# Kernel optimization log

Measured on AMD Instinct MI355X. Metric: run time of the kernel, lower is better.

## Reference

```python
import jax, jax.numpy as jnp
import numpy as np

HEADS = 8
DIM_HEAD = 64


def setup_inputs() -> dict:
    key = jax.random.key(0)
    ks = jax.random.split(key, 6)
    B, Nq, Nk, Dq = 4, 2048, 2048, 1024
    inner = HEADS * DIM_HEAD  # 512
    return {
        "x": jax.random.normal(ks[0], (B, Nq, Dq), jnp.float32),
        "context": jax.random.normal(ks[1], (B, Nk, Dq), jnp.float32),
        "Wq": jax.random.normal(ks[2], (Dq, inner), jnp.float32) * 0.02,
        "Wkv": jax.random.normal(ks[3], (Dq, 2 * inner), jnp.float32) * 0.02,
        "Wout": jax.random.normal(ks[4], (inner, Dq), jnp.float32) * 0.02,
        "bout": jax.random.normal(ks[5], (Dq,), jnp.float32) * 0.02,
        "topk": 64,
    }


def reference(x, context, Wq, Wkv, Wout, bout, topk):
    B, Nq, _ = x.shape
    Nk = context.shape[1]
    H, D = HEADS, DIM_HEAD
    scale = D ** -0.5

    # projections: b n (h d) -> b h n d
    q = (x @ Wq).reshape(B, Nq, H, D).transpose(0, 2, 1, 3)
    kv = context @ Wkv
    k, v = jnp.split(kv, 2, axis=-1)
    k = k.reshape(B, Nk, H, D).transpose(0, 2, 1, 3)
    v = v.reshape(B, Nk, H, D).transpose(0, 2, 1, 3)

    sim = jnp.einsum('bhid,bhjd->bhij', q, k) * scale  # [B,H,Nq,Nk]

    # top-k sparsification: keep only topk keys per query, mask rest to -max
    k_eff = min(int(topk), Nk)
    _, idx = jax.lax.top_k(sim, k_eff)  # [B,H,Nq,k_eff]
    keep = jnp.zeros(sim.shape, dtype=bool)
    bi = jnp.arange(B)[:, None, None, None]
    hi = jnp.arange(H)[None, :, None, None]
    qi = jnp.arange(Nq)[None, None, :, None]
    keep = keep.at[bi, hi, qi, idx].set(True)
    max_neg = -jnp.finfo(sim.dtype).max
    sim = jnp.where(keep, sim, max_neg)

    attn = jax.nn.softmax(sim, axis=-1)
    out = jnp.einsum('bhij,bhjd->bhid', attn, v)
    out = out.transpose(0, 2, 1, 3).reshape(B, Nq, H * D)
    return out @ Wout + bout
```

## Files before the change

kernel.cpp:

```cpp
#include <hip/hip_runtime.h>
#include <math.h>

#define BATCH 4
#define NQ 2048
#define NK 2048
#define DQ 1024
#define NHEADS 8
#define DHEAD 64
#define INNER (NHEADS*DHEAD)
#define NROWS (BATCH*NHEADS*NQ)
#define CAND_MAX 128

using frag_ab = __attribute__((ext_vector_type(8))) short;
using frag_cd = __attribute__((ext_vector_type(4))) float;
using u16x8   = __attribute__((ext_vector_type(8))) unsigned short;

static __device__ __forceinline__ unsigned short f32_to_bf16_rne(float f) {
  unsigned u = __float_as_uint(f);
  u += 0x7FFFu + ((u >> 16) & 1u);
  return (unsigned short)(u >> 16);
}

static __device__ __forceinline__ void split_trunc(float f, unsigned short& h, unsigned short& l) {
  unsigned u = __float_as_uint(f);
  h = (unsigned short)(u >> 16);
  float hf = __uint_as_float(u & 0xFFFF0000u);
  unsigned r = __float_as_uint(f - hf);
  l = (unsigned short)(r >> 16);
}

static __device__ __forceinline__ void split3(float f, unsigned short& h,
                                              unsigned short& m, unsigned short& l) {
  unsigned u = __float_as_uint(f);
  h = (unsigned short)(u >> 16);
  float hf = __uint_as_float(u & 0xFFFF0000u);
  float r1 = f - hf;
  unsigned u1 = __float_as_uint(r1);
  m = (unsigned short)(u1 >> 16);
  float mf = __uint_as_float(u1 & 0xFFFF0000u);
  float r2 = r1 - mf;
  l = (unsigned short)(__float_as_uint(r2) >> 16);
}

__global__ __launch_bounds__(256) void split_wT3(
    const float* __restrict__ W, int ldw, int coloff, int K, int N,
    unsigned short* __restrict__ TH, unsigned short* __restrict__ TM,
    unsigned short* __restrict__ TL)
{
  __shared__ float tile[32*33];
  const int k0 = blockIdx.x * 32, n0 = blockIdx.y * 32;
  const int t = threadIdx.x;
  {
    int lk = t >> 3, ln4 = (t & 7) * 4;
    const float4 v = *(const float4*)(W + (size_t)(k0 + lk)*ldw + coloff + n0 + ln4);
    tile[lk*33 + ln4+0] = v.x;
    tile[lk*33 + ln4+1] = v.y;
    tile[lk*33 + ln4+2] = v.z;
    tile[lk*33 + ln4+3] = v.w;
  }
  __syncthreads();
  int n = t >> 3, k4 = (t & 7) * 4;
  #pragma unroll
  for (int j = 0; j < 4; ++j) {
    unsigned short h, m, l;
    split3(tile[(k4+j)*33 + n], h, m, l);
    size_t o = (size_t)(n0 + n)*K + k0 + k4 + j;
    TH[o] = h; TM[o] = m; TL[o] = l;
  }
}

__global__ __launch_bounds__(256) void split_wT(
    const float* __restrict__ W, int ldw, int coloff, int K, int N,
    unsigned short* __restrict__ TH, unsigned short* __restrict__ TL)
{
  __shared__ float tile[32*33];
  const int k0 = blockIdx.x * 32, n0 = blockIdx.y * 32;
  const int t = threadIdx.x;
  {
    int lk = t >> 3, ln4 = (t & 7) * 4;
    const float4 v = *(const float4*)(W + (size_t)(k0 + lk)*ldw + coloff + n0 + ln4);
    tile[lk*33 + ln4+0] = v.x;
    tile[lk*33 + ln4+1] = v.y;
    tile[lk*33 + ln4+2] = v.z;
    tile[lk*33 + ln4+3] = v.w;
  }
  __syncthreads();
  int n = t >> 3, k4 = (t & 7) * 4;
  #pragma unroll
  for (int j = 0; j < 4; ++j) {
    unsigned short h, l;
    split_trunc(tile[(k4+j)*33 + n], h, l);
    TH[(size_t)(n0 + n)*K + k0 + k4 + j] = h;
    TL[(size_t)(n0 + n)*K + k0 + k4 + j] = l;
  }
}

__global__ __launch_bounds__(256) void gemm_mfma6_proj(
    const float* __restrict__ A,
    const unsigned short* __restrict__ BtH, const unsigned short* __restrict__ BtM,
    const unsigned short* __restrict__ BtL,
    float* __restrict__ C32,
    unsigned short* __restrict__ Hi, unsigned short* __restrict__ Lo)
{
  extern __shared__ unsigned short smp[];
  unsigned short* ah = smp;
  unsigned short* am = ah + 128*72;
  unsigned short* al = am + 128*72;
  unsigned short* bh = al + 128*72;
  unsigned short* bm = bh + 128*72;
  unsigned short* bl = bm + 128*72;

  const int t = threadIdx.x;
  const int w = t >> 6, l = t & 63;
  const int lr = l & 15, quad = l >> 4;
  const int n0 = blockIdx.x * 128, m0 = blockIdx.y * 128;

  frag_cd acc[2][8];
  #pragma unroll
  for (int ms = 0; ms < 2; ++ms)
    #pragma unroll
    for (int nt = 0; nt < 8; ++nt)
      acc[ms][nt] = (frag_cd){0.f, 0.f, 0.f, 0.f};

  for (int kt = 0; kt < DQ; kt += 64) {
    #pragma unroll
    for (int i = 0; i < 4; ++i) {
      int idx = i*256 + t;
      int row = idx >> 3, k8 = (idx & 7) * 8;
      const float* src = A + (size_t)(m0 + row) * DQ + kt + k8;
      float4 v0 = *(const float4*)(src);
      float4 v1 = *(const float4*)(src + 4);
      float vv[8] = {v0.x, v0.y, v0.z, v0.w, v1.x, v1.y, v1.z, v1.w};
      unsigned short h8[8], m8[8], l8[8];
      #pragma unroll
      for (int j = 0; j < 8; ++j) split3(vv[j], h8[j], m8[j], l8[j]);
      *(u16x8*)(ah + row*72 + k8) = *(u16x8*)h8;
      *(u16x8*)(am + row*72 + k8) = *(u16x8*)m8;
      *(u16x8*)(al + row*72 + k8) = *(u16x8*)l8;
    }
    #pragma unroll
    for (int i = 0; i < 4; ++i) {
      int idx = i*256 + t;
      int n = idx >> 3, k8 = (idx & 7) * 8;
      size_t o = (size_t)(n0 + n)*DQ + kt + k8;
      *(u16x8*)(bh + n*72 + k8) = *(const u16x8*)(BtH + o);
      *(u16x8*)(bm + n*72 + k8) = *(const u16x8*)(BtM + o);
      *(u16x8*)(bl + n*72 + k8) = *(const u16x8*)(BtL + o);
    }
    __syncthreads();
    #pragma unroll
    for (int ks = 0; ks < 2; ++ks) {
      frag_ab aH[2], aM[2], aL[2];
      #pragma unroll
      for (int ms = 0; ms < 2; ++ms) {
        int row = w*32 + ms*16 + lr;
        aH[ms] = *(const frag_ab*)(ah + row*72 + ks*32 + quad*8);
        aM[ms] = *(const frag_ab*)(am + row*72 + ks*32 + quad*8);
        aL[ms] = *(const frag_ab*)(al + row*72 + ks*32 + quad*8);
      }
      #pragma unroll
      for (int nt = 0; nt < 8; ++nt) {
        int bn = nt*16 + lr;
        frag_ab bH_ = *(const frag_ab*)(bh + bn*72 + ks*32 + quad*8);
        frag_ab bM_ = *(const frag_ab*)(bm + bn*72 + ks*32 + quad*8);
        frag_ab bL_ = *(const frag_ab*)(bl + bn*72 + ks*32 + quad*8);
        #pragma unroll
        for (int ms = 0; ms < 2; ++ms) {
          frag_cd c = acc[ms][nt];
          c = __builtin_amdgcn_mfma_f32_16x16x32_bf16(aL[ms], bH_, c, 0, 0, 0);
          c = __builtin_amdgcn_mfma_f32_16x16x32_bf16(aH[ms], bL_, c, 0, 0, 0);
          c = __builtin_amdgcn_mfma_f32_16x16x32_bf16(aM[ms], bM_, c, 0, 0, 0);
          c = __builtin_amdgcn_mfma_f32_16x16x32_bf16(aM[ms], bH_, c, 0, 0, 0);
          c = __builtin_amdgcn_mfma_f32_16x16x32_bf16(aH[ms], bM_, c, 0, 0, 0);
          c = __builtin_amdgcn_mfma_f32_16x16x32_bf16(aH[ms], bH_, c, 0, 0, 0);
          acc[ms][nt] = c;
        }
      }
    }
    __syncthreads();
  }

  #pragma unroll
  for (int ms = 0; ms < 2; ++ms)
    #pragma unroll
    for (int nt = 0; nt < 8; ++nt) {
      int cc = n0 + nt*16 + lr;
      int h = cc >> 6, d = cc & 63;
      #pragma unroll
      for (int i = 0; i < 4; ++i) {
        int r = m0 + w*32 + ms*16 + quad*4 + i;
        int b = r >> 11, n = r & (NQ - 1);
        size_t idx = (((size_t)(b*NHEADS + h))*NQ + n)*64 + d;
        float vf = acc[ms][nt][i];
        C32[idx] = vf;
        unsigned short hb = f32_to_bf16_rne(vf);
        float hf = __uint_as_float((unsigned)hb << 16);
        unsigned short lb = f32_to_bf16_rne(vf - hf);
        Hi[idx] = hb;
        Lo[idx] = lb;
      }
    }
}

template<int MODE>
__global__ __launch_bounds__(256) void gemm_mfma3(
    const float* __restrict__ A, int lda,
    const unsigned short* __restrict__ BtH, const unsigned short* __restrict__ BtL,
    int K, int N, const float* __restrict__ bias, float* __restrict__ C0)
{
  __shared__ unsigned short ah[128*72];
  __shared__ unsigned short al[128*72];
  __shared__ unsigned short bh2[64*72];
  __shared__ unsigned short bl2[64*72];
  const int t = threadIdx.x;
  const int w = t >> 6, l = t & 63;
  const int lr = l & 15, quad = l >> 4;
  const int n0 = blockIdx.x * 64, m0 = blockIdx.y * 128;

  frag_cd acc[2][4];
  #pragma unroll
  for (int ms = 0; ms < 2; ++ms)
    #pragma unroll
    for (int nt = 0; nt < 4; ++nt)
      acc[ms][nt] = (frag_cd){0.f, 0.f, 0.f, 0.f};

  for (int kt = 0; kt < K; kt += 64) {
    #pragma unroll
    for (int i = 0; i < 4; ++i) {
      int idx = i*256 + t;
      int row = idx >> 3, k8 = (idx & 7) * 8;
      const float* src = A + (size_t)(m0 + row) * lda + kt + k8;
      float4 v0 = *(const float4*)(src);
      float4 v1 = *(const float4*)(src + 4);
      float vv[8] = {v0.x, v0.y, v0.z, v0.w, v1.x, v1.y, v1.z, v1.w};
      unsigned short h8[8], l8[8];
      #pragma unroll
      for (int j = 0; j < 8; ++j) split_trunc(vv[j], h8[j], l8[j]);
      *(u16x8*)(ah + row*72 + k8) = *(u16x8*)h8;
      *(u16x8*)(al + row*72 + k8) = *(u16x8*)l8;
    }
    #pragma unroll
    for (int i = 0; i < 2; ++i) {
      int idx = i*256 + t;
      int n = idx >> 3, k8 = (idx & 7) * 8;
      *(u16x8*)(bh2 + n*72 + k8) = *(const u16x8*)(BtH + (size_t)(n0 + n)*K + kt + k8);
      *(u16x8*)(bl2 + n*72 + k8) = *(const u16x8*)(BtL + (size_t)(n0 + n)*K + kt + k8);
    }
    __syncthreads();
    #pragma unroll
    for (int ks = 0; ks < 2; ++ks) {
      frag_ab aH[2], aL[2], bH[4], bL[4];
      #pragma unroll
      for (int ms = 0; ms < 2; ++ms) {
        int row = w*32 + ms*16 + lr;
        aH[ms] = *(const frag_ab*)(ah + row*72 + ks*32 + quad*8);
        aL[ms] = *(const frag_ab*)(al + row*72 + ks*32 + quad*8);
      }
      #pragma unroll
      for (int nt = 0; nt < 4; ++nt) {
        int row = nt*16 + lr;
        bH[nt] = *(const frag_ab*)(bh2 + row*72 + ks*32 + quad*8);
        bL[nt] = *(const frag_ab*)(bl2 + row*72 + ks*32 + quad*8);
      }
      #pragma unroll
      for (int ms = 0; ms < 2; ++ms)
        #pragma unroll
        for (int nt = 0; nt < 4; ++nt) {
          acc[ms][nt] = __builtin_amdgcn_mfma_f32_16x16x32_bf16(aH[ms], bH[nt], acc[ms][nt], 0, 0, 0);
          acc[ms][nt] = __builtin_amdgcn_mfma_f32_16x16x32_bf16(aH[ms], bL[nt], acc[ms][nt], 0, 0, 0);
          acc[ms][nt] = __builtin_amdgcn_mfma_f32_16x16x32_bf16(aL[ms], bH[nt], acc[ms][nt], 0, 0, 0);
        }
    }
    __syncthreads();
  }

  #pragma unroll
  for (int ms = 0; ms < 2; ++ms)
    #pragma unroll
    for (int nt = 0; nt < 4; ++nt) {
      int cc = n0 + nt*16 + lr;
      #pragma unroll
      for (int i = 0; i < 4; ++i) {
        int r = m0 + w*32 + ms*16 + quad*4 + i;
        float v = acc[ms][nt][i];
        if (MODE == 0) {
          C0[(size_t)r * N + cc] = v + bias[cc];
        } else {
          int b = r >> 11, n = r & (NQ - 1);
          int h = cc >> 6, d = cc & 63;
          C0[(((size_t)(b*NHEADS + h))*NK + n)*64 + d] = v;
        }
      }
    }
}

__global__ __launch_bounds__(256) void score_mfma(
    const unsigned short* __restrict__ Qhi, const unsigned short* __restrict__ Qlo,
    const unsigned short* __restrict__ Khi, const unsigned short* __restrict__ Klo,
    unsigned short* __restrict__ S16, int bh0)
{
  extern __shared__ unsigned short sm[];
  unsigned short* qh = sm;
  unsigned short* ql = qh + 128*72;
  unsigned short* kh = ql + 128*72;
  unsigned short* kl = kh + 128*72;

  const int t  = threadIdx.x;
  const int qt = blockIdx.x, kt = blockIdx.y;
  const int bh = bh0 + blockIdx.z;
  const size_t qbase = ((size_t)bh*NQ + qt*128) * 64;
  const size_t kbase = ((size_t)bh*NK + kt*128) * 64;

  #pragma unroll
  for (int i = 0; i < 4; ++i) {
    int c   = t + i*256;
    int row = c >> 3, off = (c & 7) * 8;
    *(u16x8*)(qh + row*72 + off) = *(const u16x8*)(Qhi + qbase + row*64 + off);
    *(u16x8*)(ql + row*72 + off) = *(const u16x8*)(Qlo + qbase + row*64 + off);
    *(u16x8*)(kh + row*72 + off) = *(const u16x8*)(Khi + kbase + row*64 + off);
    *(u16x8*)(kl + row*72 + off) = *(const u16x8*)(Klo + kbase + row*64 + off);
  }
  __syncthreads();

  const int w = t >> 6, l = t & 63;
  const int quad = l >> 4, lr = l & 15;

  frag_ab aH[2][2], aL[2][2];
  #pragma unroll
  for (int qs = 0; qs < 2; ++qs) {
    int row = w*32 + qs*16 + lr;
    #pragma unroll
    for (int s = 0; s < 2; ++s) {
      aH[qs][s] = *(const frag_ab*)(qh + row*72 + s*32 + quad*8);
      aL[qs][s] = *(const frag_ab*)(ql + row*72 + s*32 + quad*8);
    }
  }

  for (int ks = 0; ks < 8; ++ks) {
    frag_ab bH[2], bL[2];
    int krow = ks*16 + lr;
    #pragma unroll
    for (int s = 0; s < 2; ++s) {
      bH[s] = *(const frag_ab*)(kh + krow*72 + s*32 + quad*8);
      bL[s] = *(const frag_ab*)(kl + krow*72 + s*32 + quad*8);
    }
    #pragma unroll
    for (int qs = 0; qs < 2; ++qs) {
      frag_cd c = {0.f, 0.f, 0.f, 0.f};
      #pragma unroll
      for (int s = 0; s < 2; ++s) {
        c = __builtin_amdgcn_mfma_f32_16x16x32_bf16(aH[qs][s], bH[s], c, 0, 0, 0);
        c = __builtin_amdgcn_mfma_f32_16x16x32_bf16(aH[qs][s], bL[s], c, 0, 0, 0);
        c = __builtin_amdgcn_mfma_f32_16x16x32_bf16(aL[qs][s], bH[s], c, 0, 0, 0);
      }
      int qrow = qt*128 + w*32 + qs*16 + quad*4;
      int kcol = kt*128 + ks*16 + lr;
      size_t base = ((size_t)blockIdx.z * NQ + qrow) * NK + kcol;
      #pragma unroll
      for (int i = 0; i < 4; ++i) {
        _Float16 h = (_Float16)(c[i] * 0.125f);
        S16[base + (size_t)i*NK] = __builtin_bit_cast(unsigned short, h);
      }
    }
  }
}

__global__ __launch_bounds__(256) void select_rows(
    const unsigned short* __restrict__ S16, unsigned short* __restrict__ cand,
    int* __restrict__ cnt, const int* __restrict__ topkp, int row0)
{
  const int t = threadIdx.x;
  const int w = t >> 6, l = t & 63;
  const int rl = blockIdx.x * 4 + w;
  const size_t row = (size_t)row0 + rl;
  const unsigned short* Sr = S16 + (size_t)rl * NK;
  const unsigned long long lmask = (1ull << l) - 1ull;

  int kEff = *topkp;
  if (kEff > CAND_MAX) kEff = CAND_MAX;
  if (kEff < 1) kEff = 1;

  unsigned uv[32];
  #pragma unroll
  for (int c = 0; c < 32; ++c) {
    unsigned bb = Sr[c*64 + l];
    uv[c] = (bb & 0x8000u) ? (~bb & 0xFFFFu) : (bb | 0x8000u);
  }
  unsigned lo_ = 0u, hi_ = 0xFFFFu;
  while (lo_ < hi_) {
    unsigned mid = (lo_ + hi_ + 1u) >> 1;
    int c_ = 0;
    #pragma unroll
    for (int c = 0; c < 32; ++c) c_ += (uv[c] >= mid) ? 1 : 0;
    #pragma unroll
    for (int off = 32; off > 0; off >>= 1) c_ += __shfl_xor(c_, off);
    if (c_ >= kEff) lo_ = mid; else hi_ = mid - 1;
  }
  unsigned short sb = (lo_ & 0x8000u) ? (unsigned short)(lo_ & 0x7FFFu)
                                      : (unsigned short)(~lo_ & 0xFFFFu);
  float skth = (float)__builtin_bit_cast(_Float16, sb);
  float smarg = skth - 3e-3f;
  _Float16 hm = (_Float16)smarg;
  unsigned short mb = __builtin_bit_cast(unsigned short, hm);
  unsigned um = (mb & 0x8000u) ? (~(unsigned)mb & 0xFFFFu) : ((unsigned)mb | 0x8000u);

  int base = 0;
  for (int c = 0; c < 32; ++c) {
    bool pred = (uv[c] >= um);
    unsigned long long msk = __ballot(pred);
    if (pred) {
      int pos = base + __popcll(msk & lmask);
      if (pos < CAND_MAX) cand[row*CAND_MAX + pos] = (unsigned short)(c*64 + l);
    }
    base += __popcll(msk);
  }
  if (l == 0) cnt[row] = (base < CAND_MAX) ? base : CAND_MAX;
}

__global__ __launch_bounds__(256) void attn_phase_b(
    const float* __restrict__ Q32, const float* __restrict__ K32,
    const float* __restrict__ V32, const unsigned short* __restrict__ cand,
    const int* __restrict__ cnt, float* __restrict__ inner,
    const int* __restrict__ topkp)
{
  __shared__ uint2 pvbuf[4][128];

  const int t = threadIdx.x;
  const int w = t >> 6, l = t & 63;
  const int nwg = (int)gridDim.x;
  const int bid = (int)blockIdx.x;
  const int swz = (bid & 7) * (nwg >> 3) + (bid >> 3);
  const size_t row = (size_t)swz * 4 + w;
  const int bh = (int)(row >> 11);
  const int q  = (int)(row & (NQ - 1));
  const unsigned long long lmask = (1ull << l) - 1ull;

  int kEff = *topkp;
  if (kEff > CAND_MAX) kEff = CAND_MAX;
  if (kEff < 1) kEff = 1;
  int m = cnt[row];
  if (kEff > m) kEff = m;

  const float* Kb = K32 + (size_t)bh * NK * 64;
  const float* Vb = V32 + (size_t)bh * NK * 64;

  const int g = l >> 3, r = l & 7;
  double2 q2[4];
  #pragma unroll
  for (int i = 0; i < 4; ++i) {
    float2 qf = *(const float2*)(Q32 + row*64 + i*16 + r*2);
    q2[i].x = (double)qf.x;
    q2[i].y = (double)qf.y;
  }

  int ck[2];
  ck[0] = cand[row*CAND_MAX + l];
  ck[1] = cand[row*CAND_MAX + 64 + l];
  double cs[2] = {-INFINITY, -INFINITY};
  unsigned long long cu[2] = {0ull, 0ull};

  #define RESCORE_PASS(P, C)                                                  \
  {                                                                           \
    const int j = (P)*8 + g;                                                  \
    const bool valid = (j < m);                                               \
    int key = __shfl(ck[C], j & 63);                                          \
    const float* kp = Kb + (size_t)(valid ? key : 0) * 64;                    \
    double s0 = 0.0, s1 = 0.0;                                                \
    _Pragma("unroll")                                                         \
    for (int i = 0; i < 4; ++i) {                                             \
      float2 kv = *(const float2*)(kp + i*16 + r*2);                          \
      s0 = fma((double)kv.x, q2[i].x, s0);                                    \
      s1 = fma((double)kv.y, q2[i].y, s1);                                    \
    }                                                                         \
    double s = s0 + s1;                                                       \
    s += __shfl_xor(s, 1);                                                    \
    s += __shfl_xor(s, 2);                                                    \
    s += __shfl_xor(s, 4);                                                    \
    s *= 0.125;                                                               \
    double sc = __shfl(s, (l & 7) * 8);                                       \
    const int pp = (P) & 7;                                                   \
    if ((l >> 3) == pp && ((C)*64 + pp*8 + (l & 7)) < m) {                    \
      unsigned long long b = (unsigned long long)__double_as_longlong(sc);    \
      cs[C] = sc;                                                             \
      cu[C] = (b >> 63) ? ~b : (b | 0x8000000000000000ull);                   \
    }                                                                         \
  }

  if (m <= 64) {
    #pragma unroll
    for (int p = 0; p < 8; ++p) RESCORE_PASS(p, 0)
  } else {
    #pragma unroll
    for (int p = 0; p < 8; ++p) RESCORE_PASS(p, 0)
    const int np2 = 8 + ((m - 64 + 7) >> 3);
    for (int p = 8; p < np2; ++p) RESCORE_PASS(p, 1)
  }
  #undef RESCORE_PASS

  const unsigned hu0 = (unsigned)(cu[0] >> 32), lu0 = (unsigned)cu[0];
  const unsigned hu1 = (unsigned)(cu[1] >> 32), lu1 = (unsigned)cu[1];

  unsigned T32 = 0u;
  for (int bit = 31; bit >= 0; --bit) {
    unsigned cT = T32 | (1u << bit);
    int tot = __popcll(__ballot(hu0 >= cT)) + __popcll(__ballot(hu1 >= cT));
    if (tot >= kEff) T32 = cT;
  }
  unsigned Tlo;
  {
    int cgt32 = __popcll(__ballot(hu0 > T32)) + __popcll(__ballot(hu1 > T32));
    bool e0 = (hu0 == T32), e1 = (hu1 == T32);
    unsigned long long bm0 = __ballot(e0), bm1 = __ballot(e1);
    int ceq = __popcll(bm0) + __popcll(bm1);
    int nEq32 = kEff - cgt32;
    if (ceq == 1) {
      Tlo = bm0 ? __shfl(lu0, (int)__builtin_ctzll(bm0))
                : __shfl(lu1, (int)__builtin_ctzll(bm1));
    } else {
      unsigned TL = 0u;
      for (int bit = 31; bit >= 0; --bit) {
        unsigned cT = TL | (1u << bit);
        int tot = __popcll(__ballot(e0 && lu0 >= cT))
                + __popcll(__ballot(e1 && lu1 >= cT));
        if (tot >= nEq32) TL = cT;
      }
      Tlo = TL;
    }
  }
  const unsigned long long T = ((unsigned long long)T32 << 32) | Tlo;

  double s_kth;
  { unsigned long long bb = (T >> 63) ? (T & 0x7FFFFFFFFFFFFFFFull) : ~T;
    s_kth = __longlong_as_double((long long)bb); }

  double nx = -INFINITY;
  #pragma unroll
  for (int c = 0; c < 2; ++c) { double v = (cu[c] < T) ? cs[c] : -INFINITY; nx = fmax(nx, v); }
  #pragma unroll
  for (int off = 32; off > 0; off >>= 1) nx = fmax(nx, __shfl_xor(nx, off));

  double smax = fmax(cs[0], cs[1]);
  #pragma unroll
  for (int off = 32; off > 0; off >>= 1) smax = fmax(smax, __shfl_xor(smax, off));

  const double DELTA = 5e-6;
  float wgt[2];
  if (!(s_kth - nx < 2.0*DELTA)) {
    int cgt = __popcll(__ballot(cu[0] > T)) + __popcll(__ballot(cu[1] > T));
    int nEq = kEff - cgt;
    int eqBase = 0;
    #pragma unroll
    for (int c = 0; c < 2; ++c) {
      bool eq = (cu[c] == T);
      unsigned long long eqm = __ballot(eq);
      int er = __popcll(eqm & lmask);
      bool sel = (cu[c] > T) || (eq && (eqBase + er) < nEq);
      eqBase += __popcll(eqm);
      wgt[c] = sel ? expf((float)(cs[c] - smax)) : 0.f;
    }
  } else {
    double cmid = 0.5 * (s_kth + nx);
    #pragma unroll
    for (int c = 0; c < 2; ++c) {
      double mu = 0.5 + (cs[c] - cmid) / (2.0*DELTA);
      mu = fmin(1.0, fmax(0.0, mu));
      wgt[c] = (float)mu * expf((float)(cs[c] - smax));
    }
  }

  pvbuf[w][l]      = make_uint2((unsigned)ck[0] & (NK - 1), __float_as_uint(wgt[0]));
  pvbuf[w][64 + l] = make_uint2((unsigned)ck[1] & (NK - 1), __float_as_uint(wgt[1]));
  float wsum = wgt[0] + wgt[1];
  #pragma unroll
  for (int off = 32; off > 0; off >>= 1) wsum += __shfl_xor(wsum, off);
  asm volatile("s_waitcnt lgkmcnt(0)" ::: "memory");

  const int sub = l >> 4;
  const int dl  = l & 15;
  const float* Vb4 = Vb + dl * 4;
  float ax = 0.f, ay = 0.f, az = 0.f, aw = 0.f;
  const int mm4 = (m + 3) & ~3;
  #pragma unroll 4
  for (int j0 = 0; j0 < mm4; j0 += 4) {
    uint2 p = pvbuf[w][j0 + sub];
    float wj = __uint_as_float(p.y);
    const float4 v = *(const float4*)(Vb4 + ((size_t)p.x << 6));
    ax = fmaf(wj, v.x, ax);
    ay = fmaf(wj, v.y, ay);
    az = fmaf(wj, v.z, az);
    aw = fmaf(wj, v.w, aw);
  }
  #pragma unroll
  for (int off = 32; off >= 16; off >>= 1) {
    ax += __shfl_xor(ax, off);
    ay += __shfl_xor(ay, off);
    az += __shfl_xor(az, off);
    aw += __shfl_xor(aw, off);
  }
  if (sub == 0) {
    int b = bh >> 3, h = bh & 7;
    float inv = 1.0f / wsum;
    float4 o;
    o.x = ax * inv; o.y = ay * inv; o.z = az * inv; o.w = aw * inv;
    *(float4*)(inner + ((size_t)b*NQ + q)*INNER + h*DHEAD + dl*4) = o;
  }
}

extern "C" void kernel_launch(void* const* d_in, const int* in_sizes, int n_in,
                              void* d_out, int out_size, void* d_ws, size_t ws_size,
                              hipStream_t stream)
{
  const float* x    = (const float*)d_in[0];
  const float* ctx  = (const float*)d_in[1];
  const float* Wq   = (const float*)d_in[2];
  const float* Wkv  = (const float*)d_in[3];
  const float* Wout = (const float*)d_in[4];
  const float* bout = (const float*)d_in[5];
  const int*   topk = (const int*)d_in[6];
  float* out = (float*)d_out;

  const size_t SZ = (size_t)BATCH * NHEADS * NQ * DHEAD;

  size_t off = 0;
  char* base = (char*)d_ws;
  auto take = [&](size_t bytes) { char* r = base + off; off += (bytes + 255) & ~(size_t)255; return r; };
  float* Q32 = (float*)take(SZ * sizeof(float));
  float* K32 = (float*)take(SZ * sizeof(float));
  unsigned short* cand = (unsigned short*)take((size_t)NROWS * CAND_MAX * 2);
  int* cnt = (int*)take((size_t)NROWS * sizeof(int));
  unsigned short* Qhi = (unsigned short*)take(SZ * 2);
  unsigned short* Qlo = (unsigned short*)take(SZ * 2);
  unsigned short* Khi = (unsigned short*)take(SZ * 2);
  unsigned short* Klo = (unsigned short*)take(SZ * 2);
  char* slab = base + off;

  const size_t WSZ = (size_t)INNER * DQ * 2;
  unsigned short* WqTH = (unsigned short*)(slab + 0*WSZ);
  unsigned short* WqTM = (unsigned short*)(slab + 1*WSZ);
  unsigned short* WqTL = (unsigned short*)(slab + 2*WSZ);
  unsigned short* WkTH = (unsigned short*)(slab + 3*WSZ);
  unsigned short* WkTM = (unsigned short*)(slab + 4*WSZ);
  unsigned short* WkTL = (unsigned short*)(slab + 5*WSZ);
  unsigned short* S16 = (unsigned short*)slab;
  unsigned short* WvTH = (unsigned short*)(slab + 0*WSZ);
  unsigned short* WvTL = (unsigned short*)(slab + 1*WSZ);
  unsigned short* WoTH = (unsigned short*)(slab + 2*WSZ);
  unsigned short* WoTL = (unsigned short*)(slab + 3*WSZ);
  float* V32   = (float*)Qhi;
  float* inner = (float*)Khi;

  const size_t per_bh = (size_t)NQ * NK * sizeof(unsigned short);
  size_t avail = (ws_size > off) ? (ws_size - off) : 0;
  int bhchunk = (int)(avail / per_bh);
  if (bhchunk < 1)  bhchunk = 1;
  if (bhchunk > 32) bhchunk = 32;

  const int M = BATCH * NQ;
  const int SCORE_LDS = 4 * 128 * 72 * (int)sizeof(unsigned short);
  const int PROJ_LDS  = 6 * 128 * 72 * (int)sizeof(unsigned short);
  hipFuncSetAttribute(reinterpret_cast<const void*>(score_mfma),
                      hipFuncAttributeMaxDynamicSharedMemorySize, SCORE_LDS);
  hipFuncSetAttribute(reinterpret_cast<const void*>(gemm_mfma6_proj),
                      hipFuncAttributeMaxDynamicSharedMemorySize, PROJ_LDS);

  split_wT3<<<dim3(DQ/32, INNER/32), 256, 0, stream>>>(Wq,  INNER,   0, DQ, INNER, WqTH, WqTM, WqTL);
  split_wT3<<<dim3(DQ/32, INNER/32), 256, 0, stream>>>(Wkv, 2*INNER, 0, DQ, INNER, WkTH, WkTM, WkTL);

  gemm_mfma6_proj<<<dim3(INNER/128, M/128), 256, PROJ_LDS, stream>>>(x,   WqTH, WqTM, WqTL, Q32, Qhi, Qlo);
  gemm_mfma6_proj<<<dim3(INNER/128, M/128), 256, PROJ_LDS, stream>>>(ctx, WkTH, WkTM, WkTL, K32, Khi, Klo);

  for (int c0 = 0; c0 < BATCH*NHEADS; c0 += bhchunk) {
    int cc = BATCH*NHEADS - c0; if (cc > bhchunk) cc = bhchunk;
    score_mfma<<<dim3(NQ/128, NK/128, cc), 256, SCORE_LDS, stream>>>(
        Qhi, Qlo, Khi, Klo, S16, c0);
    select_rows<<<dim3(cc*NQ/4), 256, 0, stream>>>(S16, cand, cnt, topk, c0*NQ);
  }

  split_wT<<<dim3(DQ/32, INNER/32), 256, 0, stream>>>(Wkv, 2*INNER, INNER, DQ, INNER, WvTH, WvTL);
  split_wT<<<dim3(INNER/32, DQ/32), 256, 0, stream>>>(Wout, DQ, 0, INNER, DQ, WoTH, WoTL);

  gemm_mfma3<2><<<dim3(INNER/64, M/128), 256, 0, stream>>>(ctx, DQ, WvTH, WvTL, DQ, INNER, nullptr, V32);
  attn_phase_b<<<dim3(NROWS/4), 256, 0, stream>>>(Q32, K32, V32, cand, cnt, inner, topk);
  gemm_mfma3<0><<<dim3(DQ/64, M/128), 256, 0, stream>>>(inner, INNER, WoTH, WoTL, INNER, DQ, bout, out);
}
```

Baseline: 836.9 us.

## Retile Q/K projection GEMM to 128x64 tiles, 512 threads, remapped block order

New measurement: 723.0 us. -13.6%, faster.

```diff
diff --git a/kernel.cpp b/kernel.cpp
--- a/kernel.cpp
+++ b/kernel.cpp
@@ -95,7 +95,7 @@
   }
 }
 
-__global__ __launch_bounds__(256) void gemm_mfma6_proj(
+__global__ __launch_bounds__(512) void gemm_mfma6_proj(
     const float* __restrict__ A,
     const unsigned short* __restrict__ BtH, const unsigned short* __restrict__ BtM,
     const unsigned short* __restrict__ BtL,
@@ -104,29 +104,27 @@
 {
   extern __shared__ unsigned short smp[];
   unsigned short* ah = smp;
-  unsigned short* am = ah + 128*72;
-  unsigned short* al = am + 128*72;
-  unsigned short* bh = al + 128*72;
-  unsigned short* bm = bh + 128*72;
-  unsigned short* bl = bm + 128*72;
+  unsigned short* am = ah + 128*40;
+  unsigned short* al = am + 128*40;
+  unsigned short* bh = al + 128*40;
+  unsigned short* bm = bh + 64*40;
+  unsigned short* bl = bm + 64*40;
 
   const int t = threadIdx.x;
   const int w = t >> 6, l = t & 63;
   const int lr = l & 15, quad = l >> 4;
-  const int n0 = blockIdx.x * 128, m0 = blockIdx.y * 128;
-
-  frag_cd acc[2][8];
-  #pragma unroll
-  for (int ms = 0; ms < 2; ++ms)
-    #pragma unroll
-    for (int nt = 0; nt < 8; ++nt)
-      acc[ms][nt] = (frag_cd){0.f, 0.f, 0.f, 0.f};
-
-  for (int kt = 0; kt < DQ; kt += 64) {
-    #pragma unroll
-    for (int i = 0; i < 4; ++i) {
-      int idx = i*256 + t;
-      int row = idx >> 3, k8 = (idx & 7) * 8;
+  const int bid = (int)blockIdx.x;
+  const int lid = (bid & 7) * 64 + (bid >> 3);
+  const int n0 = (lid & 7) * 64, m0 = (lid >> 3) * 128;
+
+  frag_cd acc[4];
+  #pragma unroll
+  for (int nt = 0; nt < 4; ++nt)
+    acc[nt] = (frag_cd){0.f, 0.f, 0.f, 0.f};
+
+  for (int kt = 0; kt < DQ; kt += 32) {
+    {
+      int row = t >> 2, k8 = (t & 3) * 8;
       const float* src = A + (size_t)(m0 + row) * DQ + kt + k8;
       float4 v0 = *(const float4*)(src);
       float4 v1 = *(const float4*)(src + 4);
@@ -134,72 +132,60 @@
       unsigned short h8[8], m8[8], l8[8];
       #pragma unroll
       for (int j = 0; j < 8; ++j) split3(vv[j], h8[j], m8[j], l8[j]);
-      *(u16x8*)(ah + row*72 + k8) = *(u16x8*)h8;
-      *(u16x8*)(am + row*72 + k8) = *(u16x8*)m8;
-      *(u16x8*)(al + row*72 + k8) = *(u16x8*)l8;
-    }
+      *(u16x8*)(ah + row*40 + k8) = *(u16x8*)h8;
+      *(u16x8*)(am + row*40 + k8) = *(u16x8*)m8;
+      *(u16x8*)(al + row*40 + k8) = *(u16x8*)l8;
+    }
+    if (t < 256) {
+      int n = t >> 2, k8 = (t & 3) * 8;
+      size_t o = (size_t)(n0 + n)*DQ + kt + k8;
+      *(u16x8*)(bh + n*40 + k8) = *(const u16x8*)(BtH + o);
+      *(u16x8*)(bm + n*40 + k8) = *(const u16x8*)(BtM + o);
+      *(u16x8*)(bl + n*40 + k8) = *(const u16x8*)(BtL + o);
+    }
+    __syncthreads();
+    {
+      int row = w*16 + lr;
+      frag_ab aH = *(const frag_ab*)(ah + row*40 + quad*8);
+      frag_ab aM = *(const frag_ab*)(am + row*40 + quad*8);
+      frag_ab aL = *(const frag_ab*)(al + row*40 + quad*8);
+      #pragma unroll
+      for (int nt = 0; nt < 4; ++nt) {
+        int bn = nt*16 + lr;
+        frag_ab bH_ = *(const frag_ab*)(bh + bn*40 + quad*8);
+        frag_ab bM_ = *(const frag_ab*)(bm + bn*40 + quad*8);
+        frag_ab bL_ = *(const frag_ab*)(bl + bn*40 + quad*8);
+        frag_cd c = acc[nt];
+        c = __builtin_amdgcn_mfma_f32_16x16x32_bf16(aL, bH_, c, 0, 0, 0);
+        c = __builtin_amdgcn_mfma_f32_16x16x32_bf16(aH, bL_, c, 0, 0, 0);
+        c = __builtin_amdgcn_mfma_f32_16x16x32_bf16(aM, bM_, c, 0, 0, 0);
+        c = __builtin_amdgcn_mfma_f32_16x16x32_bf16(aM, bH_, c, 0, 0, 0);
+        c = __builtin_amdgcn_mfma_f32_16x16x32_bf16(aH, bM_, c, 0, 0, 0);
+        c = __builtin_amdgcn_mfma_f32_16x16x32_bf16(aH, bH_, c, 0, 0, 0);
+        acc[nt] = c;
+      }
+    }
+    __syncthreads();
+  }
+
+  #pragma unroll
+  for (int nt = 0; nt < 4; ++nt) {
+    int cc = n0 + nt*16 + lr;
+    int h = cc >> 6, d = cc & 63;
     #pragma unroll
     for (int i = 0; i < 4; ++i) {
-      int idx = i*256 + t;
-      int n = idx >> 3, k8 = (idx & 7) * 8;
-      size_t o = (size_t)(n0 + n)*DQ + kt + k8;
-      *(u16x8*)(bh + n*72 + k8) = *(const u16x8*)(BtH + o);
-      *(u16x8*)(bm + n*72 + k8) = *(const u16x8*)(BtM + o);
-      *(u16x8*)(bl + n*72 + k8) = *(const u16x8*)(BtL + o);
-    }
-    __syncthreads();
-    #pragma unroll
-    for (int ks = 0; ks < 2; ++ks) {
-      frag_ab aH[2], aM[2], aL[2];
-      #pragma unroll
-      for (int ms = 0; ms < 2; ++ms) {
-        int row = w*32 + ms*16 + lr;
-        aH[ms] = *(const frag_ab*)(ah + row*72 + ks*32 + quad*8);
-        aM[ms] = *(const frag_ab*)(am + row*72 + ks*32 + quad*8);
-        aL[ms] = *(const frag_ab*)(al + row*72 + ks*32 + quad*8);
-      }
-      #pragma unroll
-      for (int nt = 0; nt < 8; ++nt) {
-        int bn = nt*16 + lr;
-        frag_ab bH_ = *(const frag_ab*)(bh + bn*72 + ks*32 + quad*8);
-        frag_ab bM_ = *(const frag_ab*)(bm + bn*72 + ks*32 + quad*8);
-        frag_ab bL_ = *(const frag_ab*)(bl + bn*72 + ks*32 + quad*8);
-        #pragma unroll
-        for (int ms = 0; ms < 2; ++ms) {
-          frag_cd c = acc[ms][nt];
-          c = __builtin_amdgcn_mfma_f32_16x16x32_bf16(aL[ms], bH_, c, 0, 0, 0);
-          c = __builtin_amdgcn_mfma_f32_16x16x32_bf16(aH[ms], bL_, c, 0, 0, 0);
-          c = __builtin_amdgcn_mfma_f32_16x16x32_bf16(aM[ms], bM_, c, 0, 0, 0);
-          c = __builtin_amdgcn_mfma_f32_16x16x32_bf16(aM[ms], bH_, c, 0, 0, 0);
-          c = __builtin_amdgcn_mfma_f32_16x16x32_bf16(aH[ms], bM_, c, 0, 0, 0);
-          c = __builtin_amdgcn_mfma_f32_16x16x32_bf16(aH[ms], bH_, c, 0, 0, 0);
-          acc[ms][nt] = c;
-        }
-      }
-    }
-    __syncthreads();
-  }
-
-  #pragma unroll
-  for (int ms = 0; ms < 2; ++ms)
-    #pragma unroll
-    for (int nt = 0; nt < 8; ++nt) {
-      int cc = n0 + nt*16 + lr;
-      int h = cc >> 6, d = cc & 63;
-      #pragma unroll
-      for (int i = 0; i < 4; ++i) {
-        int r = m0 + w*32 + ms*16 + quad*4 + i;
-        int b = r >> 11, n = r & (NQ - 1);
-        size_t idx = (((size_t)(b*NHEADS + h))*NQ + n)*64 + d;
-        float vf = acc[ms][nt][i];
-        C32[idx] = vf;
-        unsigned short hb = f32_to_bf16_rne(vf);
-        float hf = __uint_as_float((unsigned)hb << 16);
-        unsigned short lb = f32_to_bf16_rne(vf - hf);
-        Hi[idx] = hb;
-        Lo[idx] = lb;
-      }
-    }
+      int r = m0 + w*16 + quad*4 + i;
+      int b = r >> 11, n = r & (NQ - 1);
+      size_t idx = (((size_t)(b*NHEADS + h))*NQ + n)*64 + d;
+      float vf = acc[nt][i];
+      C32[idx] = vf;
+      unsigned short hb = f32_to_bf16_rne(vf);
+      float hf = __uint_as_float((unsigned)hb << 16);
+      unsigned short lb = f32_to_bf16_rne(vf - hf);
+      Hi[idx] = hb;
+      Lo[idx] = lb;
+    }
+  }
 }
 
 template<int MODE>
@@ -657,7 +643,7 @@
 
   const int M = BATCH * NQ;
   const int SCORE_LDS = 4 * 128 * 72 * (int)sizeof(unsigned short);
-  const int PROJ_LDS  = 6 * 128 * 72 * (int)sizeof(unsigned short);
+  const int PROJ_LDS  = 6 * 64 * 40 * (int)sizeof(unsigned short) * 2;
   hipFuncSetAttribute(reinterpret_cast<const void*>(score_mfma),
                       hipFuncAttributeMaxDynamicSharedMemorySize, SCORE_LDS);
   hipFuncSetAttribute(reinterpret_cast<const void*>(gemm_mfma6_proj),
@@ -666,8 +652,8 @@
   split_wT3<<<dim3(DQ/32, INNER/32), 256, 0, stream>>>(Wq,  INNER,   0, DQ, INNER, WqTH, WqTM, WqTL);
   split_wT3<<<dim3(DQ/32, INNER/32), 256, 0, stream>>>(Wkv, 2*INNER, 0, DQ, INNER, WkTH, WkTM, WkTL);
 
-  gemm_mfma6_proj<<<dim3(INNER/128, M/128), 256, PROJ_LDS, stream>>>(x,   WqTH, WqTM, WqTL, Q32, Qhi, Qlo);
-  gemm_mfma6_proj<<<dim3(INNER/128, M/128), 256, PROJ_LDS, stream>>>(ctx, WkTH, WkTM, WkTL, K32, Khi, Klo);
+  gemm_mfma6_proj<<<dim3((INNER/64)*(M/128)), 512, PROJ_LDS, stream>>>(x,   WqTH, WqTM, WqTL, Q32, Qhi, Qlo);
+  gemm_mfma6_proj<<<dim3((INNER/64)*(M/128)), 512, PROJ_LDS, stream>>>(ctx, WkTH, WkTM, WkTL, K32, Khi, Klo);
 
   for (int c0 = 0; c0 < BATCH*NHEADS; c0 += bhchunk) {
     int cc = BATCH*NHEADS - c0; if (cc > bhchunk) cc = bhchunk;
```
